# Kernel optimization log

Hardware: AMD Instinct MI355X
Metric: run time of the kernel (lower is better)

Reference implementation:

```python
import jax, jax.numpy as jnp
import numpy as np

N_NODES = 40000
N_EDGES = 640000
D_FEAT = 128
HIDDEN = 128
N_GRAPHS = 512


def setup_inputs() -> dict:
    key = jax.random.key(0)
    ks = jax.random.split(key, 6)
    x = jax.random.normal(ks[0], (N_NODES, D_FEAT), dtype=jnp.float32)
    edge_index = jax.random.randint(ks[1], (2, N_EDGES), 0, N_NODES, dtype=jnp.int32)
    batch = jnp.sort(jax.random.randint(ks[2], (N_NODES,), 0, N_GRAPHS, dtype=jnp.int32))
    s1 = 1.0 / np.sqrt(D_FEAT)
    s2 = 1.0 / np.sqrt(HIDDEN)
    W1 = jax.random.normal(ks[3], (D_FEAT, HIDDEN), dtype=jnp.float32) * s1
    b1 = jnp.zeros((HIDDEN,), dtype=jnp.float32)
    W2 = jax.random.normal(ks[4], (HIDDEN, HIDDEN), dtype=jnp.float32) * s2
    b2 = jnp.zeros((HIDDEN,), dtype=jnp.float32)
    Wfc = jax.random.normal(ks[5], (HIDDEN, 1), dtype=jnp.float32) * s2
    bfc = jnp.zeros((1,), dtype=jnp.float32)
    return {"x": x, "edge_index": edge_index, "batch": batch,
            "W1": W1, "b1": b1, "W2": W2, "b2": b2, "Wfc": Wfc, "bfc": bfc}


def _gcn_conv(x, edge_index, W, b):
    # PyG GCNConv: linear transform, add self-loops, symmetric deg^{-1/2} norm,
    # scatter-add messages from row (source) to col (target), then bias.
    n = x.shape[0]
    h = x @ W  # [N, H]
    row, col = edge_index[0], edge_index[1]
    ones = jnp.ones_like(col, dtype=h.dtype)
    deg = 1.0 + jax.ops.segment_sum(ones, col, num_segments=n)  # self-loop included
    dinv = jax.lax.rsqrt(deg)  # [N]
    norm = dinv[row] * dinv[col]  # [E]
    msg = h[row] * norm[:, None]  # [E, H]
    out = jax.ops.segment_sum(msg, col, num_segments=n)
    out = out + h * (dinv * dinv)[:, None]  # self-loop contribution
    return out + b


def _mean_pool(x, batch, num_graphs):
    sums = jax.ops.segment_sum(x, batch, num_segments=num_graphs)
    cnt = jax.ops.segment_sum(jnp.ones((x.shape[0],), dtype=x.dtype), batch, num_segments=num_graphs)
    return sums / jnp.maximum(cnt, 1.0)[:, None]


def reference(x, edge_index, batch, W1, b1, W2, b2, Wfc, bfc):
    h = jax.nn.relu(_gcn_conv(x, edge_index, W1, b1))
    h = jax.nn.relu(_gcn_conv(h, edge_index, W2, b2))
    g = _mean_pool(h, batch, N_GRAPHS)  # [G, H]
    return g @ Wfc + bfc  # [G, 1]
```

## Files before the change

kernel.cpp:

```cpp
#include <hip/hip_runtime.h>
#include <hip/hip_fp16.h>

#define N_NODES 40000
#define N_EDGES 640000
#define NFEAT   128
#define N_GRAPHS 512
#define SCAN_NB 157
#define NBKT    157
#define BKT_CAP 8192
#define BIN_BLK_EDGES 2048
#define NBLK_A ((N_EDGES + BIN_BLK_EDGES - 1) / BIN_BLK_EDGES)
#define EPAD_MAX (N_EDGES + 3 * N_NODES)

__global__ void init_misc_kernel(int* __restrict__ gcursor, int* __restrict__ gcnt,
                                 float* __restrict__ out, const float* __restrict__ bfc,
                                 __half* __restrict__ hsent) {
    int t = threadIdx.x;
    if (t <= NBKT) gcursor[t] = 0;
    float b = bfc[0];
    for (int i = t; i < N_GRAPHS; i += 256) { gcnt[i] = 0; out[i] = b; }
    if (t < NFEAT) hsent[t] = __float2half(0.0f);
}

__global__ void batch_hist_kernel(const int* __restrict__ batch, int* __restrict__ gcnt, int n) {
    int i = blockIdx.x * blockDim.x + threadIdx.x;
    if (i < n) atomicAdd(&gcnt[batch[i]], 1);
}

__global__ __launch_bounds__(256) void bin_kernel(const int* __restrict__ ei,
                                                  int* __restrict__ gcursor,
                                                  unsigned int* __restrict__ binned) {
    __shared__ int lhist[NBKT];
    __shared__ int lbase[NBKT];
    const int t  = threadIdx.x;
    const int e0 = blockIdx.x * BIN_BLK_EDGES;

    if (t < NBKT) lhist[t] = 0;
    __syncthreads();

    int creg[BIN_BLK_EDGES / 256];
    #pragma unroll
    for (int i = 0; i < BIN_BLK_EDGES / 256; ++i) {
        int e = e0 + i * 256 + t;
        creg[i] = (e < N_EDGES) ? ei[N_EDGES + e] : -1;
        if (creg[i] >= 0) atomicAdd(&lhist[creg[i] >> 8], 1);
    }
    __syncthreads();

    if (t < NBKT) { lbase[t] = atomicAdd(&gcursor[t], lhist[t]); lhist[t] = 0; }
    __syncthreads();

    #pragma unroll
    for (int i = 0; i < BIN_BLK_EDGES / 256; ++i) {
        int c = creg[i];
        if (c >= 0) {
            int e = e0 + i * 256 + t;
            int r = ei[e];
            int bkt = c >> 8;
            int slot = atomicAdd(&lhist[bkt], 1);
            binned[(size_t)bkt * BKT_CAP + lbase[bkt] + slot] =
                (unsigned int)r | ((unsigned int)(c & 255) << 16);
        }
    }
}

template <typename IdxT>
__global__ __launch_bounds__(256) void bucket_build_kernel(const unsigned int* __restrict__ binned,
                                                           const int* __restrict__ gcursor,
                                                           int* __restrict__ gbase,
                                                           float* __restrict__ dinv,
                                                           int* __restrict__ rowptr,
                                                           IdxT* __restrict__ csr) {
    __shared__ int chist[256];
    __shared__ int scn[256];
    __shared__ int ccur[256];
    __shared__ int sbase;
    const int b = blockIdx.x, t = threadIdx.x;
    chist[t] = 0;
    __syncthreads();
    const int cnt = gcursor[b];
    const unsigned int* src = binned + (size_t)b * BKT_CAP;
    for (int i = t; i < cnt; i += 256) atomicAdd(&chist[src[i] >> 16], 1);
    __syncthreads();
    const int col = b * 256 + t;
    const int valid = (col < N_NODES);
    int d = chist[t];
    if (valid) dinv[col] = rsqrtf(1.0f + (float)d);
    int pd = valid ? ((d + 3) & ~3) : 0;
    scn[t] = pd;
    __syncthreads();
    for (int off = 1; off < 256; off <<= 1) {
        int add = (t >= off) ? scn[t - off] : 0;
        __syncthreads();
        scn[t] += add;
        __syncthreads();
    }
    if (t == 255) sbase = atomicAdd(gbase, scn[255]);
    __syncthreads();
    const int start = sbase + scn[t] - pd;
    if (valid) rowptr[col] = start | ((pd >> 2) << 20);
    ccur[t] = start;
    __syncthreads();
    for (int i = t; i < cnt; i += 256) {
        unsigned int u = src[i];
        int slot = atomicAdd(&ccur[u >> 16], 1);
        csr[slot] = (IdxT)(u & 0xFFFFu);
    }
    __syncthreads();
    if (valid) {
        int cur = ccur[t];
        int endp = start + pd;
        for (int p = cur; p < endp; ++p) csr[p] = (IdxT)N_NODES;
    }
}

__device__ inline float4 load_h4(const __half* p) {
    uint2 raw = *(const uint2*)p;
    __half2 h0 = *(__half2*)&raw.x;
    __half2 h1 = *(__half2*)&raw.y;
    float2 f0 = __half22float2(h0);
    float2 f1 = __half22float2(h1);
    return make_float4(f0.x, f0.y, f1.x, f1.y);
}
__device__ inline float4 load4v(const float* p)  { return *(const float4*)(p); }
__device__ inline float4 load4v(const __half* p) { return load_h4(p); }

__device__ inline void acc8(const uint4& raw, float* a) {
    float2 f;
    f = __half22float2(*(const __half2*)&raw.x); a[0] += f.x; a[1] += f.y;
    f = __half22float2(*(const __half2*)&raw.y); a[2] += f.x; a[3] += f.y;
    f = __half22float2(*(const __half2*)&raw.z); a[4] += f.x; a[5] += f.y;
    f = __half22float2(*(const __half2*)&raw.w); a[6] += f.x; a[7] += f.y;
}

template <typename InT>
__global__ __launch_bounds__(256, 4) void gemm64h_kernel(const InT* __restrict__ X,
                                                         const float* __restrict__ W,
                                                         const float* __restrict__ dinv,
                                                         __half* __restrict__ H) {
    __shared__ float Ws[128 * 64];
    const int colhalf = blockIdx.x & 1;
    const int tile    = blockIdx.x >> 1;

    for (int i = threadIdx.x; i < 2048; i += 256) {
        int k   = i >> 4;
        int cc4 = (i & 15) * 4;
        *(float4*)(Ws + k * 64 + cc4) = *(const float4*)(W + k * 128 + colhalf * 64 + cc4);
    }
    __syncthreads();

    const int rg = threadIdx.x >> 4;
    const int cg = threadIdx.x & 15;
    const int row0 = tile * 64 + rg * 4;
    const InT* x0 = X + (size_t)row0 * NFEAT;

    float acc[4][4] = {};
    float4 xc[4], xn[4];
    #pragma unroll
    for (int i = 0; i < 4; i++) xc[i] = load4v(x0 + (size_t)i * NFEAT);

    #pragma unroll 4
    for (int k = 0; k < 128; k += 4) {
        const int kn = (k + 4) & 127;
        #pragma unroll
        for (int i = 0; i < 4; i++) xn[i] = load4v(x0 + (size_t)i * NFEAT + kn);

        float4 wv[4];
        #pragma unroll
        for (int m = 0; m < 4; m++) wv[m] = *(const float4*)(Ws + (k + m) * 64 + cg * 4);

        #pragma unroll
        for (int i = 0; i < 4; i++) {
            const float xi[4] = {xc[i].x, xc[i].y, xc[i].z, xc[i].w};
            #pragma unroll
            for (int m = 0; m < 4; m++) {
                acc[i][0] += xi[m] * wv[m].x;
                acc[i][1] += xi[m] * wv[m].y;
                acc[i][2] += xi[m] * wv[m].z;
                acc[i][3] += xi[m] * wv[m].w;
            }
        }
        #pragma unroll
        for (int i = 0; i < 4; i++) xc[i] = xn[i];
    }

    #pragma unroll
    for (int i = 0; i < 4; i++) {
        float dr = dinv[row0 + i];
        __half2 p0 = __floats2half2_rn(acc[i][0] * dr, acc[i][1] * dr);
        __half2 p1 = __floats2half2_rn(acc[i][2] * dr, acc[i][3] * dr);
        uint2 pk;
        pk.x = *(unsigned int*)&p0;
        pk.y = *(unsigned int*)&p1;
        *(uint2*)(H + (size_t)(row0 + i) * NFEAT + colhalf * 64 + cg * 4) = pk;
    }
}

template <typename IdxT, typename IdxV, bool FUSE_POOL>
__global__ __launch_bounds__(256) void gather_w16_kernel(
        const int* __restrict__ rowptr, const IdxT* __restrict__ csr,
        const float* __restrict__ dinv, const __half* __restrict__ Ht,
        const float* __restrict__ bias, __half* __restrict__ outh,
        const float* __restrict__ Wfc, float* __restrict__ nodedot, int n) {
    int gid  = blockIdx.x * blockDim.x + threadIdx.x;
    int node = gid >> 6;
    if (node >= n) return;
    int lane = threadIdx.x & 63;
    int q    = lane >> 4;
    int fo   = lane & 15;

    unsigned int u = (unsigned int)rowptr[node];
    int start = (int)(u & 0xFFFFFu);
    int pd    = (int)(u >> 20) << 2;
    int end   = start + pd;

    float a[8] = {0.f, 0.f, 0.f, 0.f, 0.f, 0.f, 0.f, 0.f};

    if (q == 0) {
        uint4 raw = *(const uint4*)(Ht + (size_t)node * NFEAT + fo * 8);
        acc8(raw, a);
    }

    if (start < end) {
        IdxV nxt = *(const IdxV*)(csr + start);
        for (int j = start; j < end; j += 4) {
            IdxV cur = nxt;
            int jn = j + 4;
            if (jn < end) nxt = *(const IdxV*)(csr + jn);
            int r = (q == 0) ? (int)cur.x : (q == 1) ? (int)cur.y
                  : (q == 2) ? (int)cur.z : (int)cur.w;
            uint4 raw = *(const uint4*)(Ht + (size_t)r * NFEAT + fo * 8);
            acc8(raw, a);
        }
    }

    #pragma unroll
    for (int i = 0; i < 8; i++) {
        a[i] += __shfl_xor(a[i], 16, 64);
        a[i] += __shfl_xor(a[i], 32, 64);
    }

    float di = dinv[node];
    const float4 bb0 = *(const float4*)(bias + fo * 8);
    const float4 bb1 = *(const float4*)(bias + fo * 8 + 4);
    float o0 = fmaxf(a[0] * di + bb0.x, 0.0f);
    float o1 = fmaxf(a[1] * di + bb0.y, 0.0f);
    float o2 = fmaxf(a[2] * di + bb0.z, 0.0f);
    float o3 = fmaxf(a[3] * di + bb0.w, 0.0f);
    float o4 = fmaxf(a[4] * di + bb1.x, 0.0f);
    float o5 = fmaxf(a[5] * di + bb1.y, 0.0f);
    float o6 = fmaxf(a[6] * di + bb1.z, 0.0f);
    float o7 = fmaxf(a[7] * di + bb1.w, 0.0f);

    if (!FUSE_POOL) {
        if (q == 0) {
            __half2 p0 = __floats2half2_rn(o0, o1);
            __half2 p1 = __floats2half2_rn(o2, o3);
            __half2 p2 = __floats2half2_rn(o4, o5);
            __half2 p3 = __floats2half2_rn(o6, o7);
            uint4 pk;
            pk.x = *(unsigned int*)&p0;
            pk.y = *(unsigned int*)&p1;
            pk.z = *(unsigned int*)&p2;
            pk.w = *(unsigned int*)&p3;
            *(uint4*)(outh + (size_t)node * NFEAT + fo * 8) = pk;
        }
    } else {
        const float4 wf0 = *(const float4*)(Wfc + fo * 8);
        const float4 wf1 = *(const float4*)(Wfc + fo * 8 + 4);
        float dsum = o0 * wf0.x + o1 * wf0.y + o2 * wf0.z + o3 * wf0.w
                   + o4 * wf1.x + o5 * wf1.y + o6 * wf1.z + o7 * wf1.w;
        dsum += __shfl_xor(dsum, 1, 64);
        dsum += __shfl_xor(dsum, 2, 64);
        dsum += __shfl_xor(dsum, 4, 64);
        dsum += __shfl_xor(dsum, 8, 64);
        if (lane == 0) nodedot[node] = dsum;
    }
}

__global__ void pool_final_kernel(const float* __restrict__ nodedot,
                                  const int* __restrict__ batch,
                                  const int* __restrict__ gcnt,
                                  float* __restrict__ out, int n) {
    int i = blockIdx.x * blockDim.x + threadIdx.x;
    if (i < n) {
        int g = batch[i];
        int c = gcnt[g];
        float cf = (float)(c > 0 ? c : 1);
        atomicAdd(&out[g], nodedot[i] / cf);
    }
}

__global__ void edge_deg_int_kernel(const int* __restrict__ ei, int* __restrict__ degcnt, int E) {
    int e = blockIdx.x * blockDim.x + threadIdx.x;
    if (e < E) atomicAdd(&degcnt[ei[E + e]], 1);
}

__global__ void dinv_from_int_kernel(const int* __restrict__ degcnt, float* __restrict__ dinv, int n) {
    int i = blockIdx.x * blockDim.x + threadIdx.x;
    if (i < n) dinv[i] = rsqrtf(1.0f + (float)degcnt[i]);
}

__global__ __launch_bounds__(256, 4) void gemm64f_kernel(const float* __restrict__ X,
                                                         const float* __restrict__ W,
                                                         const float* __restrict__ dinv,
                                                         float* __restrict__ H) {
    __shared__ float Ws[128 * 64];
    const int colhalf = blockIdx.x & 1;
    const int tile    = blockIdx.x >> 1;
    for (int i = threadIdx.x; i < 2048; i += 256) {
        int k   = i >> 4;
        int cc4 = (i & 15) * 4;
        *(float4*)(Ws + k * 64 + cc4) = *(const float4*)(W + k * 128 + colhalf * 64 + cc4);
    }
    __syncthreads();
    const int rg = threadIdx.x >> 4;
    const int cg = threadIdx.x & 15;
    const int row0 = tile * 64 + rg * 4;
    const float* x0 = X + (size_t)row0 * NFEAT;
    float acc[4][4] = {};
    #pragma unroll 4
    for (int k = 0; k < 128; k += 4) {
        float4 xv[4];
        float4 wv[4];
        #pragma unroll
        for (int i = 0; i < 4; i++) xv[i] = *(const float4*)(x0 + (size_t)i * NFEAT + k);
        #pragma unroll
        for (int m = 0; m < 4; m++) wv[m] = *(const float4*)(Ws + (k + m) * 64 + cg * 4);
        #pragma unroll
        for (int i = 0; i < 4; i++) {
            const float xi[4] = {xv[i].x, xv[i].y, xv[i].z, xv[i].w};
            #pragma unroll
            for (int m = 0; m < 4; m++) {
                acc[i][0] += xi[m] * wv[m].x;
                acc[i][1] += xi[m] * wv[m].y;
                acc[i][2] += xi[m] * wv[m].z;
                acc[i][3] += xi[m] * wv[m].w;
            }
        }
    }
    #pragma unroll
    for (int i = 0; i < 4; i++) {
        float dr = dinv[row0 + i];
        float4 o = {acc[i][0] * dr, acc[i][1] * dr, acc[i][2] * dr, acc[i][3] * dr};
        *(float4*)(H + (size_t)(row0 + i) * NFEAT + cg * 4 + colhalf * 64) = o;
    }
}

__global__ __launch_bounds__(256) void edge_scatter_kernel(const int* __restrict__ ei,
                                                           const float* __restrict__ dinv,
                                                           const float* __restrict__ H,
                                                           float* __restrict__ agg,
                                                           int E) {
    long long gid = (long long)blockIdx.x * blockDim.x + threadIdx.x;
    int e = (int)(gid >> 5);
    if (e >= E) return;
    int c4 = ((int)gid & 31) * 4;
    int r = ei[e];
    int c = ei[E + e];
    float norm = dinv[c];
    const float4 hv = *(const float4*)(H + (size_t)r * NFEAT + c4);
    float* dst = agg + (size_t)c * NFEAT + c4;
    atomicAdd(dst + 0, hv.x * norm);
    atomicAdd(dst + 1, hv.y * norm);
    atomicAdd(dst + 2, hv.z * norm);
    atomicAdd(dst + 3, hv.w * norm);
}

__global__ void post_kernel(float* __restrict__ agg, const float* __restrict__ H,
                            const float* __restrict__ dinv, const float* __restrict__ b,
                            int n) {
    int gid = blockIdx.x * blockDim.x + threadIdx.x;
    if (gid >= n * 32) return;
    int node = gid >> 5;
    int c4 = (gid & 31) * 4;
    float s = dinv[node];
    float4 a  = *(float4*)(agg + (size_t)gid * 4);
    float4 hv = *(const float4*)(H + (size_t)gid * 4);
    float4 bb = *(const float4*)(b + c4);
    float4 o;
    o.x = fmaxf(a.x + hv.x * s + bb.x, 0.0f);
    o.y = fmaxf(a.y + hv.y * s + bb.y, 0.0f);
    o.z = fmaxf(a.z + hv.z * s + bb.z, 0.0f);
    o.w = fmaxf(a.w + hv.w * s + bb.w, 0.0f);
    *(float4*)(agg + (size_t)gid * 4) = o;
}

__global__ __launch_bounds__(128) void pool_fc_kernel(const float* __restrict__ H,
                                                      const int* __restrict__ batch,
                                                      const float* __restrict__ Wfc,
                                                      const float* __restrict__ bfc,
                                                      float* __restrict__ out, int n) {
    int g = blockIdx.x;
    int tid = threadIdx.x;
    int lo = 0, hi = n;
    while (lo < hi) { int mid = (lo + hi) >> 1; if (batch[mid] < g) lo = mid + 1; else hi = mid; }
    int start = lo;
    hi = n;
    while (lo < hi) { int mid = (lo + hi) >> 1; if (batch[mid] < g + 1) lo = mid + 1; else hi = mid; }
    int end = lo;
    float acc = 0.0f;
    for (int nd = start; nd < end; ++nd) acc += H[(size_t)nd * NFEAT + tid];
    float cnt = (float)((end - start) > 0 ? (end - start) : 1);
    float v = (acc / cnt) * Wfc[tid];
    __shared__ float red[128];
    red[tid] = v;
    __syncthreads();
    #pragma unroll
    for (int s = 64; s > 0; s >>= 1) {
        if (tid < s) red[tid] += red[tid + s];
        __syncthreads();
    }
    if (tid == 0) out[g] = red[0] + bfc[0];
}

static void run_csr_path(const float* x, const int* ei, const int* batch,
                         const float* W1, const float* b1, const float* W2,
                         const float* b2, const float* Wfc, const float* bfc,
                         float* out, void* d_ws, hipStream_t stream) {
    typedef unsigned short IdxT;
    typedef ushort4 IdxV;
    char* ws = (char*)d_ws;
    const size_t hbytes = (size_t)(N_NODES + 1) * NFEAT * sizeof(__half);
    const size_t obytes = (size_t)N_NODES * NFEAT * sizeof(__half);
    __half* hbuf  = (__half*)ws;
    __half* obuf  = (__half*)(ws + hbytes);
    IdxT*   csr   = (IdxT*)(ws + hbytes + obytes);
    char*   p     = ws + hbytes + obytes + ((size_t)EPAD_MAX * sizeof(IdxT) + 15) / 16 * 16;
    int*    rowptr = (int*)p;                p += ((size_t)(N_NODES + 1) * 4 + 15) / 16 * 16;
    float*  dinv   = (float*)p;              p += ((size_t)N_NODES * 4 + 15) / 16 * 16;
    int*    gcnt   = (int*)p;

    unsigned int* binned = (unsigned int*)obuf;
    int* gcursor = (int*)(binned + (size_t)NBKT * BKT_CAP);
    float* nodedot = (float*)(p + (((size_t)N_GRAPHS * 4 + 15) / 16 * 16));

    init_misc_kernel<<<1, 256, 0, stream>>>(gcursor, gcnt, out, bfc,
                                            hbuf + (size_t)N_NODES * NFEAT);
    batch_hist_kernel<<<SCAN_NB, 256, 0, stream>>>(batch, gcnt, N_NODES);
    bin_kernel<<<NBLK_A, 256, 0, stream>>>(ei, gcursor, binned);
    bucket_build_kernel<IdxT><<<NBKT, 256, 0, stream>>>(binned, gcursor, gcursor + NBKT,
                                                        dinv, rowptr, csr);

    gemm64h_kernel<float><<<(N_NODES / 64) * 2, 256, 0, stream>>>(x, W1, dinv, hbuf);
    gather_w16_kernel<IdxT, IdxV, false><<<(N_NODES * 64) / 256, 256, 0, stream>>>(
        rowptr, csr, dinv, hbuf, b1, obuf, nullptr, nullptr, N_NODES);

    gemm64h_kernel<__half><<<(N_NODES / 64) * 2, 256, 0, stream>>>(obuf, W2, dinv, hbuf);
    gather_w16_kernel<IdxT, IdxV, true><<<(N_NODES * 64) / 256, 256, 0, stream>>>(
        rowptr, csr, dinv, hbuf, b2, nullptr, Wfc, nodedot, N_NODES);

    pool_final_kernel<<<SCAN_NB, 256, 0, stream>>>(nodedot, batch, gcnt, out, N_NODES);
}

extern "C" void kernel_launch(void* const* d_in, const int* in_sizes, int n_in,
                              void* d_out, int out_size, void* d_ws, size_t ws_size,
                              hipStream_t stream) {
    const float* x     = (const float*)d_in[0];
    const int*   ei    = (const int*)  d_in[1];
    const int*   batch = (const int*)  d_in[2];
    const float* W1    = (const float*)d_in[3];
    const float* b1    = (const float*)d_in[4];
    const float* W2    = (const float*)d_in[5];
    const float* b2    = (const float*)d_in[6];
    const float* Wfc   = (const float*)d_in[7];
    const float* bfc   = (const float*)d_in[8];
    float* out = (float*)d_out;

    const size_t hbytes = (size_t)(N_NODES + 1) * NFEAT * sizeof(__half);
    const size_t obytes = (size_t)N_NODES * NFEAT * sizeof(__half);
    const size_t tail   = ((size_t)(N_NODES + 1) * 4 + 15) / 16 * 16
                        + ((size_t)N_NODES * 4 + 15) / 16 * 16
                        + (((size_t)N_GRAPHS * 4 + 15) / 16 * 16)
                        + (size_t)N_NODES * 4;
    const size_t need = hbytes + obytes + ((size_t)EPAD_MAX * 2 + 15) / 16 * 16 + tail;

    if (ws_size >= need) {
        run_csr_path(x, ei, batch, W1, b1, W2, b2, Wfc, bfc, out, d_ws, stream);
    } else {
        float* ws   = (float*)d_ws;
        int*   degc = (int*)ws;
        float* dinv = ws + N_NODES;
        float* hbuf = ws + 2 * N_NODES;
        float* agg  = hbuf + (size_t)N_NODES * NFEAT;
        const size_t fb2 = (size_t)N_NODES * NFEAT * sizeof(float);

        hipMemsetAsync(degc, 0, (size_t)N_NODES * sizeof(int), stream);
        edge_deg_int_kernel<<<N_EDGES / 256, 256, 0, stream>>>(ei, degc, N_EDGES);
        dinv_from_int_kernel<<<SCAN_NB, 256, 0, stream>>>(degc, dinv, N_NODES);

        hipMemsetAsync(agg, 0, fb2, stream);
        gemm64f_kernel<<<(N_NODES / 64) * 2, 256, 0, stream>>>(x, W1, dinv, hbuf);
        edge_scatter_kernel<<<(N_EDGES * 32) / 256, 256, 0, stream>>>(ei, dinv, hbuf, agg, N_EDGES);
        post_kernel<<<(N_NODES * 32) / 256, 256, 0, stream>>>(agg, hbuf, dinv, b1, N_NODES);

        gemm64f_kernel<<<(N_NODES / 64) * 2, 256, 0, stream>>>(agg, W2, dinv, hbuf);
        hipMemsetAsync(agg, 0, fb2, stream);
        edge_scatter_kernel<<<(N_EDGES * 32) / 256, 256, 0, stream>>>(ei, dinv, hbuf, agg, N_EDGES);
        post_kernel<<<(N_NODES * 32) / 256, 256, 0, stream>>>(agg, hbuf, dinv, b2, N_NODES);

        pool_fc_kernel<<<N_GRAPHS, 128, 0, stream>>>(agg, batch, Wfc, bfc, out, N_NODES);
    }
}
```

Baseline: 266.7 us.

## Fuse graph histogram and pooling into CSR build and gather, unroll gather by eight

The per-graph node histogram moves into the bucket-build kernel as a shared-memory histogram, and the final mean-pool atomic moves into the second gather kernel. This removes two separate launches and the nodedot buffer. The gather loop now takes eight neighbours per iteration, with rows padded to multiples of 8, giving two independent row loads in flight; the node index and rowptr are read via readfirstlane so they stay scalar. The extra padding adds more sentinel-row loads per node, and the pooling now issues one atomic per node from inside the gather.

```diff
diff --git a/kernel.cpp b/kernel.cpp
--- a/kernel.cpp
+++ b/kernel.cpp
@@ -10,7 +10,7 @@
 #define BKT_CAP 8192
 #define BIN_BLK_EDGES 2048
 #define NBLK_A ((N_EDGES + BIN_BLK_EDGES - 1) / BIN_BLK_EDGES)
-#define EPAD_MAX (N_EDGES + 3 * N_NODES)
+#define EPAD_MAX (N_EDGES + 7 * N_NODES)
 
 __global__ void init_misc_kernel(int* __restrict__ gcursor, int* __restrict__ gcnt,
                                  float* __restrict__ out, const float* __restrict__ bfc,
@@ -20,11 +20,6 @@
     float b = bfc[0];
     for (int i = t; i < N_GRAPHS; i += 256) { gcnt[i] = 0; out[i] = b; }
     if (t < NFEAT) hsent[t] = __float2half(0.0f);
-}
-
-__global__ void batch_hist_kernel(const int* __restrict__ batch, int* __restrict__ gcnt, int n) {
-    int i = blockIdx.x * blockDim.x + threadIdx.x;
-    if (i < n) atomicAdd(&gcnt[batch[i]], 1);
 }
 
 __global__ __launch_bounds__(256) void bin_kernel(const int* __restrict__ ei,
@@ -68,25 +63,31 @@
 __global__ __launch_bounds__(256) void bucket_build_kernel(const unsigned int* __restrict__ binned,
                                                            const int* __restrict__ gcursor,
                                                            int* __restrict__ gbase,
+                                                           const int* __restrict__ batch,
+                                                           int* __restrict__ gcnt,
                                                            float* __restrict__ dinv,
                                                            int* __restrict__ rowptr,
                                                            IdxT* __restrict__ csr) {
     __shared__ int chist[256];
     __shared__ int scn[256];
     __shared__ int ccur[256];
+    __shared__ int ghist[N_GRAPHS];
     __shared__ int sbase;
     const int b = blockIdx.x, t = threadIdx.x;
     chist[t] = 0;
+    ghist[t] = 0;
+    ghist[t + 256] = 0;
     __syncthreads();
     const int cnt = gcursor[b];
     const unsigned int* src = binned + (size_t)b * BKT_CAP;
-    for (int i = t; i < cnt; i += 256) atomicAdd(&chist[src[i] >> 16], 1);
-    __syncthreads();
     const int col = b * 256 + t;
     const int valid = (col < N_NODES);
+    if (valid) atomicAdd(&ghist[batch[col]], 1);
+    for (int i = t; i < cnt; i += 256) atomicAdd(&chist[src[i] >> 16], 1);
+    __syncthreads();
     int d = chist[t];
     if (valid) dinv[col] = rsqrtf(1.0f + (float)d);
-    int pd = valid ? ((d + 3) & ~3) : 0;
+    int pd = valid ? ((d + 7) & ~7) : 0;
     scn[t] = pd;
     __syncthreads();
     for (int off = 1; off < 256; off <<= 1) {
@@ -112,6 +113,9 @@
         int endp = start + pd;
         for (int p = cur; p < endp; ++p) csr[p] = (IdxT)N_NODES;
     }
+    int h0 = ghist[t], h1 = ghist[t + 256];
+    if (h0) atomicAdd(&gcnt[t], h0);
+    if (h1) atomicAdd(&gcnt[t + 256], h1);
 }
 
 __device__ inline float4 load_h4(const __half* p) {
@@ -131,6 +135,12 @@
     f = __half22float2(*(const __half2*)&raw.y); a[2] += f.x; a[3] += f.y;
     f = __half22float2(*(const __half2*)&raw.z); a[4] += f.x; a[5] += f.y;
     f = __half22float2(*(const __half2*)&raw.w); a[6] += f.x; a[7] += f.y;
+}
+
+__device__ inline int pick_q(ushort4 v, int q) {
+    unsigned long long ul;
+    __builtin_memcpy(&ul, &v, 8);
+    return (int)((unsigned int)(ul >> (q << 4)) & 0xFFFFu);
 }
 
 template <typename InT>
@@ -201,15 +211,16 @@
         const int* __restrict__ rowptr, const IdxT* __restrict__ csr,
         const float* __restrict__ dinv, const __half* __restrict__ Ht,
         const float* __restrict__ bias, __half* __restrict__ outh,
-        const float* __restrict__ Wfc, float* __restrict__ nodedot, int n) {
+        const float* __restrict__ Wfc, const int* __restrict__ batch,
+        const int* __restrict__ gcnt, float* __restrict__ out, int n) {
     int gid  = blockIdx.x * blockDim.x + threadIdx.x;
-    int node = gid >> 6;
+    int node = __builtin_amdgcn_readfirstlane(gid >> 6);
     if (node >= n) return;
     int lane = threadIdx.x & 63;
     int q    = lane >> 4;
     int fo   = lane & 15;
 
-    unsigned int u = (unsigned int)rowptr[node];
+    unsigned int u = (unsigned int)__builtin_amdgcn_readfirstlane(rowptr[node]);
     int start = (int)(u & 0xFFFFFu);
     int pd    = (int)(u >> 20) << 2;
     int end   = start + pd;
@@ -222,15 +233,21 @@
     }
 
     if (start < end) {
-        IdxV nxt = *(const IdxV*)(csr + start);
-        for (int j = start; j < end; j += 4) {
-            IdxV cur = nxt;
-            int jn = j + 4;
-            if (jn < end) nxt = *(const IdxV*)(csr + jn);
-            int r = (q == 0) ? (int)cur.x : (q == 1) ? (int)cur.y
-                  : (q == 2) ? (int)cur.z : (int)cur.w;
-            uint4 raw = *(const uint4*)(Ht + (size_t)r * NFEAT + fo * 8);
-            acc8(raw, a);
+        IdxV n0 = *(const IdxV*)(csr + start);
+        IdxV n1 = *(const IdxV*)(csr + start + 4);
+        for (int j = start; j < end; j += 8) {
+            IdxV c0 = n0, c1 = n1;
+            int jn = j + 8;
+            if (jn < end) {
+                n0 = *(const IdxV*)(csr + jn);
+                n1 = *(const IdxV*)(csr + jn + 4);
+            }
+            int ra = pick_q(c0, q);
+            int rb = pick_q(c1, q);
+            uint4 raw0 = *(const uint4*)(Ht + (size_t)ra * NFEAT + fo * 8);
+            uint4 raw1 = *(const uint4*)(Ht + (size_t)rb * NFEAT + fo * 8);
+            acc8(raw0, a);
+            acc8(raw1, a);
         }
     }
 
@@ -274,20 +291,12 @@
         dsum += __shfl_xor(dsum, 2, 64);
         dsum += __shfl_xor(dsum, 4, 64);
         dsum += __shfl_xor(dsum, 8, 64);
-        if (lane == 0) nodedot[node] = dsum;
-    }
-}
-
-__global__ void pool_final_kernel(const float* __restrict__ nodedot,
-                                  const int* __restrict__ batch,
-                                  const int* __restrict__ gcnt,
-                                  float* __restrict__ out, int n) {
-    int i = blockIdx.x * blockDim.x + threadIdx.x;
-    if (i < n) {
-        int g = batch[i];
-        int c = gcnt[g];
-        float cf = (float)(c > 0 ? c : 1);
-        atomicAdd(&out[g], nodedot[i] / cf);
+        if (lane == 0) {
+            int g = batch[node];
+            int c = gcnt[g];
+            float cf = (float)(c > 0 ? c : 1);
+            atomicAdd(&out[g], dsum / cf);
+        }
     }
 }
 
@@ -433,24 +442,20 @@
 
     unsigned int* binned = (unsigned int*)obuf;
     int* gcursor = (int*)(binned + (size_t)NBKT * BKT_CAP);
-    float* nodedot = (float*)(p + (((size_t)N_GRAPHS * 4 + 15) / 16 * 16));
 
     init_misc_kernel<<<1, 256, 0, stream>>>(gcursor, gcnt, out, bfc,
                                             hbuf + (size_t)N_NODES * NFEAT);
-    batch_hist_kernel<<<SCAN_NB, 256, 0, stream>>>(batch, gcnt, N_NODES);
     bin_kernel<<<NBLK_A, 256, 0, stream>>>(ei, gcursor, binned);
     bucket_build_kernel<IdxT><<<NBKT, 256, 0, stream>>>(binned, gcursor, gcursor + NBKT,
-                                                        dinv, rowptr, csr);
+                                                        batch, gcnt, dinv, rowptr, csr);
 
     gemm64h_kernel<float><<<(N_NODES / 64) * 2, 256, 0, stream>>>(x, W1, dinv, hbuf);
     gather_w16_kernel<IdxT, IdxV, false><<<(N_NODES * 64) / 256, 256, 0, stream>>>(
-        rowptr, csr, dinv, hbuf, b1, obuf, nullptr, nullptr, N_NODES);
+        rowptr, csr, dinv, hbuf, b1, obuf, nullptr, nullptr, nullptr, nullptr, N_NODES);
 
     gemm64h_kernel<__half><<<(N_NODES / 64) * 2, 256, 0, stream>>>(obuf, W2, dinv, hbuf);
     gather_w16_kernel<IdxT, IdxV, true><<<(N_NODES * 64) / 256, 256, 0, stream>>>(
-        rowptr, csr, dinv, hbuf, b2, nullptr, Wfc, nodedot, N_NODES);
-
-    pool_final_kernel<<<SCAN_NB, 256, 0, stream>>>(nodedot, batch, gcnt, out, N_NODES);
+        rowptr, csr, dinv, hbuf, b2, nullptr, Wfc, batch, gcnt, out, N_NODES);
 }
 
 extern "C" void kernel_launch(void* const* d_in, const int* in_sizes, int n_in,
@@ -471,8 +476,7 @@
     const size_t obytes = (size_t)N_NODES * NFEAT * sizeof(__half);
     const size_t tail   = ((size_t)(N_NODES + 1) * 4 + 15) / 16 * 16
                         + ((size_t)N_NODES * 4 + 15) / 16 * 16
-                        + (((size_t)N_GRAPHS * 4 + 15) / 16 * 16)
-                        + (size_t)N_NODES * 4;
+                        + (size_t)N_GRAPHS * 4;
     const size_t need = hbytes + obytes + ((size_t)EPAD_MAX * 2 + 15) / 16 * 16 + tail;
 
     if (ws_size >= need) {
```

Result: slower. 276.5 us (+3.7%).
